# Kernel tuning notes

Measured on AMD Instinct MI355X. Metric: run time of the kernel, lower is better.

Reference implementation:

```python
import jax, jax.numpy as jnp
import numpy as np

B, C_CLS, D_WORD, J = 1024, 80, 300, 8000
IMG_CH = 2048

def setup_inputs() -> dict:
    key = jax.random.key(0)
    ks = jax.random.split(key, 9)
    return {
        'feature': jax.random.normal(ks[0], (B, IMG_CH), jnp.float32),
        'inp': jax.random.normal(ks[1], (1, C_CLS, D_WORD), jnp.float32),
        'A': jax.random.uniform(ks[2], (C_CLS, C_CLS), jnp.float32),
        'W_gc1': jax.random.normal(ks[3], (D_WORD, 1024), jnp.float32) * (1.0 / np.sqrt(1024)),
        'W_gc2': jax.random.normal(ks[4], (1024, 2048), jnp.float32) * (1.0 / np.sqrt(2048)),
        'W_img': jax.random.normal(ks[5], (J, IMG_CH), jnp.float32) * 0.02,
        'b_img': jax.random.normal(ks[6], (J,), jnp.float32) * 0.02,
        'W_cls': jax.random.normal(ks[7], (J, 2048), jnp.float32) * 0.02,
        'b_cls': jax.random.normal(ks[8], (J,), jnp.float32) * 0.02,
    }

def _gen_adj(A):
    # torch: D = A.sum(1)**-0.5; adj = (A @ diag(D)).T @ diag(D) = D[:,None]*A.T*D[None,:]
    D = jnp.power(jnp.sum(A, axis=1), -0.5)
    return D[:, None] * A.T * D[None, :]

def reference(feature, inp, A, W_gc1, W_gc2, W_img, b_img, W_cls, b_cls):
    inp0 = inp[0]                                   # [C, 300]
    adj = jax.lax.stop_gradient(_gen_adj(A))        # [C, C], .detach() in torch
    x = adj @ (inp0 @ W_gc1)                        # gc1: [C, 1024]
    x = jax.nn.leaky_relu(x, negative_slope=0.2)
    x = adj @ (x @ W_gc2)                           # gc2: [C, 2048]
    # MFB bilinear pooling (is_usemfb=True, is_hash=False -> out_in_tmp=1, eval-mode dropout=identity)
    # original: out[b,c] = sum_j (Linear_img(feature[b])[j] * Linear_cls(x_col_c)[j])
    img_proj = feature @ W_img.T + b_img            # [B, J]
    cls_proj = x @ W_cls.T + b_cls                  # [C, J]
    x_out = img_proj @ cls_proj.T                   # [B, C]
    return x_out
```

## Files before the change

kernel.cpp:

```cpp
#include <hip/hip_runtime.h>
#include <hip/hip_bf16.h>


typedef __bf16 bf16_t;
typedef __bf16 bf16x8 __attribute__((ext_vector_type(8)));
typedef float f32x4 __attribute__((ext_vector_type(4)));

#define MFMA16(a, b, c) __builtin_amdgcn_mfma_f32_16x16x32_bf16((a), (b), (c), 0, 0, 0)

__device__ inline bf16x8 cvt8(float4 a, float4 b) {
  bf16x8 v;
  v[0] = (bf16_t)a.x; v[1] = (bf16_t)a.y; v[2] = (bf16_t)a.z; v[3] = (bf16_t)a.w;
  v[4] = (bf16_t)b.x; v[5] = (bf16_t)b.y; v[6] = (bf16_t)b.z; v[7] = (bf16_t)b.w;
  return v;
}

__global__ void k_adj(const float* __restrict__ A, float* __restrict__ adj) {
  __shared__ float Dv[80];
  int tid = threadIdx.x;
  if (tid < 80) {
    float s = 0.f;
    #pragma unroll 4
    for (int j = 0; j < 80; ++j) s += A[tid * 80 + j];
    Dv[tid] = rsqrtf(s);
  }
  __syncthreads();
  for (int idx = tid; idx < 6400; idx += blockDim.x) {
    int i = idx / 80, j = idx % 80;
    adj[idx] = Dv[i] * Dv[j] * A[j * 80 + i];
  }
}

__global__ void k_cvt0(const float* __restrict__ inp0, bf16_t* __restrict__ x0b) {
  int idx = blockIdx.x * blockDim.x + threadIdx.x;
  if (idx < 30720) {
    int c = idx / 384, k = idx % 384;
    x0b[idx] = (k < 300) ? (bf16_t)inp0[c * 300 + k] : (bf16_t)0.f;
  }
}

__global__ __launch_bounds__(256) void k_gc1m(
    const bf16_t* __restrict__ x0b, const float* __restrict__ Wgc1,
    float* __restrict__ t1) {
  int tid = threadIdx.x;
  int w = tid >> 6, l = tid & 63;
  int ln = l & 15, q = l >> 4;
  int n0 = blockIdx.x * 16;

  __shared__ float red[4][80][16];
  f32x4 acc[5] = {};
  for (int ks = 0; ks < 3; ++ks) {
    int kq = w * 96 + ks * 32 + q * 8;
    bf16x8 bfrag;
    #pragma unroll
    for (int jj = 0; jj < 8; ++jj) {
      int k = kq + jj;
      int kc = k < 300 ? k : 299;
      float wv = Wgc1[kc * 1024 + n0 + ln];
      bfrag[jj] = (bf16_t)(k < 300 ? wv : 0.f);
    }
    #pragma unroll
    for (int mt = 0; mt < 5; ++mt) {
      bf16x8 afrag = *(const bf16x8*)(x0b + (size_t)(mt * 16 + ln) * 384 + kq);
      acc[mt] = MFMA16(afrag, bfrag, acc[mt]);
    }
  }
  #pragma unroll
  for (int mt = 0; mt < 5; ++mt)
    #pragma unroll
    for (int reg = 0; reg < 4; ++reg)
      red[w][mt * 16 + q * 4 + reg][ln] = acc[mt][reg];
  __syncthreads();
  for (int o = tid; o < 1280; o += 256) {
    int c = o >> 4, nn = o & 15;
    t1[c * 1024 + n0 + nn] = red[0][c][nn] + red[1][c][nn] + red[2][c][nn] + red[3][c][nn];
  }
}

__global__ void k_adjmul_leaky(const float* __restrict__ adj, const float* __restrict__ t1,
                               bf16_t* __restrict__ x1b) {
  int idx = blockIdx.x * blockDim.x + threadIdx.x;
  int c = idx >> 10, n = idx & 1023;
  const float* ar = adj + c * 80;
  float acc = 0.f;
  #pragma unroll 4
  for (int cc = 0; cc < 80; ++cc) acc += ar[cc] * t1[cc * 1024 + n];
  x1b[idx] = (bf16_t)(acc > 0.f ? acc : 0.2f * acc);
}

__global__ __launch_bounds__(256) void k_gc2m(
    const bf16_t* __restrict__ x1b, const float* __restrict__ Wgc2,
    float* __restrict__ t2) {
  int tid = threadIdx.x;
  int w = tid >> 6, l = tid & 63;
  int ln = l & 15, q = l >> 4;
  int nc = blockIdx.x & 31, kc = blockIdx.x >> 5;

  __shared__ float Bs[32][66];
  f32x4 acc[5] = {};
  for (int s = 0; s < 2; ++s) {
    int k0 = kc * 64 + s * 32;
    #pragma unroll
    for (int it = 0; it < 2; ++it) {
      int slot = tid + it * 256;
      int kr = slot >> 4, nq = slot & 15;
      const float4 v = *(const float4*)(Wgc2 + (size_t)(k0 + kr) * 2048 + nc * 64 + nq * 4);
      *(float4*)&Bs[kr][nq * 4] = v;
    }
    __syncthreads();
    bf16x8 bfrag;
    #pragma unroll
    for (int jj = 0; jj < 8; ++jj) bfrag[jj] = (bf16_t)Bs[q * 8 + jj][w * 16 + ln];
    #pragma unroll
    for (int mt = 0; mt < 5; ++mt) {
      bf16x8 afrag = *(const bf16x8*)(x1b + (size_t)(mt * 16 + ln) * 1024 + k0 + q * 8);
      acc[mt] = MFMA16(afrag, bfrag, acc[mt]);
    }
    __syncthreads();
  }
  #pragma unroll
  for (int mt = 0; mt < 5; ++mt)
    #pragma unroll
    for (int reg = 0; reg < 4; ++reg)
      atomicAdd(&t2[(size_t)(mt * 16 + q * 4 + reg) * 2048 + nc * 64 + w * 16 + ln],
                acc[mt][reg]);
}

__global__ void k_adjmul_bf16(const float* __restrict__ adj, const float* __restrict__ t2,
                              bf16_t* __restrict__ x2) {
  int idx = blockIdx.x * blockDim.x + threadIdx.x;
  int c = idx >> 11, n = idx & 2047;
  const float* ar = adj + c * 80;
  float acc = 0.f;
  #pragma unroll 4
  for (int cc = 0; cc < 80; ++cc) acc += ar[cc] * t2[cc * 2048 + n];
  x2[idx] = (bf16_t)acc;
}

__global__ __launch_bounds__(256) void k_clsproj(
    const float* __restrict__ Wcls, const float* __restrict__ bcls,
    const float* __restrict__ bimg, const bf16_t* __restrict__ x2,
    bf16_t* __restrict__ P, float* __restrict__ r) {
  int tid = threadIdx.x;
  int w = tid >> 6, l = tid & 63;
  int ln = l & 15, q = l >> 4;
  int j0 = blockIdx.x * 16;
  size_t jrow = (size_t)(j0 + ln) * 2048;

  __shared__ float red[4][80][16];
  __shared__ float rloc[80];
  if (tid < 80) rloc[tid] = 0.f;

  f32x4 acc[5] = {};
  int kbase = w * 512 + q * 8;
  for (int ks = 0; ks < 16; ++ks) {
    int kq = kbase + ks * 32;
    const float4* bp = (const float4*)(Wcls + jrow + kq);
    float4 b0 = bp[0], b1 = bp[1];
    bf16x8 bfrag = cvt8(b0, b1);
    #pragma unroll
    for (int mt = 0; mt < 5; ++mt) {
      bf16x8 afrag = *(const bf16x8*)(x2 + (size_t)(mt * 16 + ln) * 2048 + kq);
      acc[mt] = MFMA16(afrag, bfrag, acc[mt]);
    }
  }
  #pragma unroll
  for (int mt = 0; mt < 5; ++mt)
    #pragma unroll
    for (int reg = 0; reg < 4; ++reg)
      red[w][mt * 16 + q * 4 + reg][ln] = acc[mt][reg];
  __syncthreads();

  for (int o = tid; o < 1280; o += 256) {
    int c = o >> 4, jj = o & 15;
    float v = red[0][c][jj] + red[1][c][jj] + red[2][c][jj] + red[3][c][jj] + bcls[j0 + jj];
    P[(size_t)c * 8000 + j0 + jj] = (bf16_t)v;
    atomicAdd(&rloc[c], bimg[j0 + jj] * v);
  }
  __syncthreads();
  if (tid < 80) atomicAdd(&r[tid], rloc[tid]);
}

__global__ __launch_bounds__(256) void k_hmat(
    const float* __restrict__ Wimg, const bf16_t* __restrict__ P, float* __restrict__ H) {
  int tid = threadIdx.x;
  int w = tid >> 6, l = tid & 63;
  int ln = l & 15, q = l >> 4;
  int nc = blockIdx.x & 31, jc = blockIdx.x >> 5;

  __shared__ float Bs[32][66];
  f32x4 acc[5] = {};
  for (int s = 0; s < 10; ++s) {
    int j0 = jc * 320 + s * 32;
    #pragma unroll
    for (int it = 0; it < 2; ++it) {
      int slot = tid + it * 256;
      int jr = slot >> 4, nq = slot & 15;
      const float4 v = *(const float4*)(Wimg + (size_t)(j0 + jr) * 2048 + nc * 64 + nq * 4);
      *(float4*)&Bs[jr][nq * 4] = v;
    }
    __syncthreads();
    bf16x8 bfrag;
    #pragma unroll
    for (int jj = 0; jj < 8; ++jj) bfrag[jj] = (bf16_t)Bs[q * 8 + jj][w * 16 + ln];
    #pragma unroll
    for (int mt = 0; mt < 5; ++mt) {
      bf16x8 afrag = *(const bf16x8*)(P + (size_t)(mt * 16 + ln) * 8000 + j0 + q * 8);
      acc[mt] = MFMA16(afrag, bfrag, acc[mt]);
    }
    __syncthreads();
  }
  #pragma unroll
  for (int mt = 0; mt < 5; ++mt)
    #pragma unroll
    for (int reg = 0; reg < 4; ++reg)
      atomicAdd(&H[(size_t)(mt * 16 + q * 4 + reg) * 2048 + nc * 64 + w * 16 + ln],
                acc[mt][reg]);
}

__global__ __launch_bounds__(256) void k_out(
    const float* __restrict__ feat, const float* __restrict__ H,
    const float* __restrict__ r, float* __restrict__ out) {
  int tid = threadIdx.x;
  int w = tid >> 6, l = tid & 63;
  int ln = l & 15, q = l >> 4;
  int mg = blockIdx.x & 15, kc = blockIdx.x >> 4;
  int m0 = mg * 64 + w * 16;
  size_t frow = (size_t)(m0 + ln) * 2048;

  f32x4 acc[5] = {};
  int kbase = kc * 256 + q * 8;
  for (int ks = 0; ks < 8; ++ks) {
    int kq = kbase + ks * 32;
    const float4* ap = (const float4*)(feat + frow + kq);
    bf16x8 afrag = cvt8(ap[0], ap[1]);
    #pragma unroll
    for (int nt = 0; nt < 5; ++nt) {
      const float4* hp = (const float4*)(H + (size_t)(nt * 16 + ln) * 2048 + kq);
      bf16x8 bfrag = cvt8(hp[0], hp[1]);
      acc[nt] = MFMA16(afrag, bfrag, acc[nt]);
    }
  }
  #pragma unroll
  for (int nt = 0; nt < 5; ++nt)
    #pragma unroll
    for (int reg = 0; reg < 4; ++reg) {
      int b = m0 + q * 4 + reg;
      int c = nt * 16 + ln;
      float v = acc[nt][reg];
      if (kc == 0) v += r[c];
      atomicAdd(&out[b * 80 + c], v);
    }
}

extern "C" void kernel_launch(void* const* d_in, const int* in_sizes, int n_in,
                              void* d_out, int out_size, void* d_ws, size_t ws_size,
                              hipStream_t stream) {
  const float* feature = (const float*)d_in[0];
  const float* inp     = (const float*)d_in[1];
  const float* A       = (const float*)d_in[2];
  const float* Wgc1    = (const float*)d_in[3];
  const float* Wgc2    = (const float*)d_in[4];
  const float* Wimg    = (const float*)d_in[5];
  const float* bimg    = (const float*)d_in[6];
  const float* Wcls    = (const float*)d_in[7];
  const float* bcls    = (const float*)d_in[8];
  float* out = (float*)d_out;

  char* ws = (char*)d_ws;
  float*  adj = (float*)(ws + 0);
  float*  t1  = (float*)(ws + 25600);
  bf16_t* x1b = (bf16_t*)(ws + 353280);
  float*  t2  = (float*)(ws + 517120);
  bf16_t* x2  = (bf16_t*)(ws + 1172480);
  bf16_t* P   = (bf16_t*)(ws + 1500160);
  float*  H   = (float*)(ws + 2780160);
  float*  r   = (float*)(ws + 3435520);
  bf16_t* x0b = (bf16_t*)(ws + 3435840);

  hipMemsetAsync(t2, 0, 80 * 2048 * 4, stream);
  hipMemsetAsync(H, 0, 80 * 2048 * 4, stream);
  hipMemsetAsync(r, 0, 80 * 4, stream);
  hipMemsetAsync(out, 0, 1024 * 80 * 4, stream);

  k_adj<<<1, 128, 0, stream>>>(A, adj);
  k_cvt0<<<120, 256, 0, stream>>>(inp, x0b);
  k_gc1m<<<64, 256, 0, stream>>>(x0b, Wgc1, t1);
  k_adjmul_leaky<<<320, 256, 0, stream>>>(adj, t1, x1b);
  k_gc2m<<<512, 256, 0, stream>>>(x1b, Wgc2, t2);
  k_adjmul_bf16<<<640, 256, 0, stream>>>(adj, t2, x2);
  k_clsproj<<<500, 256, 0, stream>>>(Wcls, bcls, bimg, x2, P, r);
  k_hmat<<<800, 256, 0, stream>>>(Wimg, P, H);
  k_out<<<128, 256, 0, stream>>>(feature, H, r, out);
}
```

Before: 280.8 us.

## Pipeline weight tiles via direct global-to-LDS loads and split k_out K

k_gc2m and k_hmat now stage their fp32 weight tiles with global_load_lds into double- and triple-buffered shared memory. Explicit vmcnt waits and barriers let the next tile's loads overlap the current tile's MFMAs, and the A fragments are prefetched into registers. k_out splits K four times finer and launches 512 blocks instead of 128 to improve occupancy, at the cost of more output atomics. The hand-tuned vmcnt counts are fragile: a miscount could read stale LDS.

```diff
diff --git a/kernel.cpp b/kernel.cpp
--- a/kernel.cpp
+++ b/kernel.cpp
@@ -7,6 +7,24 @@
 typedef float f32x4 __attribute__((ext_vector_type(4)));
 
 #define MFMA16(a, b, c) __builtin_amdgcn_mfma_f32_16x16x32_bf16((a), (b), (c), 0, 0, 0)
+
+#define GLOAD_LDS16(g, l)                                     \
+  __builtin_amdgcn_global_load_lds(                           \
+      (const __attribute__((address_space(1))) void*)(g),     \
+      (__attribute__((address_space(3))) void*)(l), 16, 0, 0)
+
+#define PIN()                                   \
+  do {                                          \
+    asm volatile("" ::: "memory");              \
+    __builtin_amdgcn_sched_barrier(0);          \
+  } while (0)
+
+#define BARRIER()                               \
+  do {                                          \
+    PIN();                                      \
+    __builtin_amdgcn_s_barrier();               \
+    PIN();                                      \
+  } while (0)
 
 __device__ inline bf16x8 cvt8(float4 a, float4 b) {
   bf16x8 v;
@@ -96,28 +114,54 @@
   int ln = l & 15, q = l >> 4;
   int nc = blockIdx.x & 31, kc = blockIdx.x >> 5;
 
-  __shared__ float Bs[32][66];
-  f32x4 acc[5] = {};
-  for (int s = 0; s < 2; ++s) {
-    int k0 = kc * 64 + s * 32;
+  __shared__ float BsF[2 * 2048];
+  auto stage = [&](int b, int k0) {
     #pragma unroll
     for (int it = 0; it < 2; ++it) {
       int slot = tid + it * 256;
       int kr = slot >> 4, nq = slot & 15;
-      const float4 v = *(const float4*)(Wgc2 + (size_t)(k0 + kr) * 2048 + nc * 64 + nq * 4);
-      *(float4*)&Bs[kr][nq * 4] = v;
-    }
-    __syncthreads();
+      const float* src = Wgc2 + (size_t)(k0 + kr) * 2048 + nc * 64 + nq * 4;
+      float* dst = BsF + b * 2048 + slot * 4;
+      GLOAD_LDS16(src, dst);
+    }
+  };
+
+  int kb = kc * 64;
+  bf16x8 a0[5], a1[5];
+  #pragma unroll
+  for (int mt = 0; mt < 5; ++mt)
+    a0[mt] = *(const bf16x8*)(x1b + (size_t)(mt * 16 + ln) * 1024 + kb + q * 8);
+  PIN();
+  stage(0, kb);
+  PIN();
+  stage(1, kb + 32);
+  PIN();
+  #pragma unroll
+  for (int mt = 0; mt < 5; ++mt)
+    a1[mt] = *(const bf16x8*)(x1b + (size_t)(mt * 16 + ln) * 1024 + kb + 32 + q * 8);
+  PIN();
+
+  f32x4 acc[5] = {};
+  asm volatile("s_waitcnt vmcnt(7)" ::: "memory");
+  BARRIER();
+  {
     bf16x8 bfrag;
     #pragma unroll
-    for (int jj = 0; jj < 8; ++jj) bfrag[jj] = (bf16_t)Bs[q * 8 + jj][w * 16 + ln];
-    #pragma unroll
-    for (int mt = 0; mt < 5; ++mt) {
-      bf16x8 afrag = *(const bf16x8*)(x1b + (size_t)(mt * 16 + ln) * 1024 + k0 + q * 8);
-      acc[mt] = MFMA16(afrag, bfrag, acc[mt]);
-    }
-    __syncthreads();
-  }
+    for (int jj = 0; jj < 8; ++jj) bfrag[jj] = (bf16_t)BsF[(q * 8 + jj) * 64 + w * 16 + ln];
+    #pragma unroll
+    for (int mt = 0; mt < 5; ++mt) acc[mt] = MFMA16(a0[mt], bfrag, acc[mt]);
+  }
+  asm volatile("s_waitcnt vmcnt(5)" ::: "memory");
+  BARRIER();
+  {
+    bf16x8 bfrag;
+    #pragma unroll
+    for (int jj = 0; jj < 8; ++jj)
+      bfrag[jj] = (bf16_t)BsF[2048 + (q * 8 + jj) * 64 + w * 16 + ln];
+    #pragma unroll
+    for (int mt = 0; mt < 5; ++mt) acc[mt] = MFMA16(a1[mt], bfrag, acc[mt]);
+  }
+
   #pragma unroll
   for (int mt = 0; mt < 5; ++mt)
     #pragma unroll
@@ -187,29 +231,64 @@
   int w = tid >> 6, l = tid & 63;
   int ln = l & 15, q = l >> 4;
   int nc = blockIdx.x & 31, jc = blockIdx.x >> 5;
-
-  __shared__ float Bs[32][66];
-  f32x4 acc[5] = {};
-  for (int s = 0; s < 10; ++s) {
-    int j0 = jc * 320 + s * 32;
+  int jbase = jc * 320;
+
+  __shared__ float BsF[3 * 2048];
+
+  auto stage = [&](int b, int j0) {
     #pragma unroll
     for (int it = 0; it < 2; ++it) {
       int slot = tid + it * 256;
       int jr = slot >> 4, nq = slot & 15;
-      const float4 v = *(const float4*)(Wimg + (size_t)(j0 + jr) * 2048 + nc * 64 + nq * 4);
-      *(float4*)&Bs[jr][nq * 4] = v;
-    }
-    __syncthreads();
+      const float* src = Wimg + (size_t)(j0 + jr) * 2048 + nc * 64 + nq * 4;
+      float* dst = BsF + b * 2048 + slot * 4;
+      GLOAD_LDS16(src, dst);
+    }
+  };
+  auto loadA = [&](bf16x8* a, int j0) {
+    #pragma unroll
+    for (int mt = 0; mt < 5; ++mt)
+      a[mt] = *(const bf16x8*)(P + (size_t)(mt * 16 + ln) * 8000 + j0 + q * 8);
+  };
+
+  f32x4 acc[5] = {};
+  bf16x8 aCur[5], aNxt[5];
+
+  loadA(aCur, jbase);
+  PIN();
+  stage(0, jbase);
+  PIN();
+  stage(1, jbase + 32);
+  PIN();
+
+  #pragma unroll
+  for (int s = 0; s < 10; ++s) {
+    if (s < 9) {
+      loadA(aNxt, jbase + (s + 1) * 32);
+      PIN();
+    }
+    if (s < 8) {
+      stage((s + 2) % 3, jbase + (s + 2) * 32);
+      PIN();
+    }
+    if (s == 0)      asm volatile("s_waitcnt vmcnt(9)"  ::: "memory");
+    else if (s < 8)  asm volatile("s_waitcnt vmcnt(14)" ::: "memory");
+    else if (s == 8) asm volatile("s_waitcnt vmcnt(12)" ::: "memory");
+    else             asm volatile("s_waitcnt vmcnt(5)"  ::: "memory");
+    BARRIER();
+    const float* Bc = BsF + (s % 3) * 2048;
     bf16x8 bfrag;
     #pragma unroll
-    for (int jj = 0; jj < 8; ++jj) bfrag[jj] = (bf16_t)Bs[q * 8 + jj][w * 16 + ln];
-    #pragma unroll
-    for (int mt = 0; mt < 5; ++mt) {
-      bf16x8 afrag = *(const bf16x8*)(P + (size_t)(mt * 16 + ln) * 8000 + j0 + q * 8);
-      acc[mt] = MFMA16(afrag, bfrag, acc[mt]);
-    }
-    __syncthreads();
-  }
+    for (int jj = 0; jj < 8; ++jj) bfrag[jj] = (bf16_t)Bc[(q * 8 + jj) * 64 + w * 16 + ln];
+    #pragma unroll
+    for (int mt = 0; mt < 5; ++mt) acc[mt] = MFMA16(aCur[mt], bfrag, acc[mt]);
+    BARRIER();
+    if (s < 9) {
+      #pragma unroll
+      for (int mt = 0; mt < 5; ++mt) aCur[mt] = aNxt[mt];
+    }
+  }
+
   #pragma unroll
   for (int mt = 0; mt < 5; ++mt)
     #pragma unroll
@@ -229,8 +308,9 @@
   size_t frow = (size_t)(m0 + ln) * 2048;
 
   f32x4 acc[5] = {};
-  int kbase = kc * 256 + q * 8;
-  for (int ks = 0; ks < 8; ++ks) {
+  int kbase = kc * 64 + q * 8;
+  #pragma unroll
+  for (int ks = 0; ks < 2; ++ks) {
     int kq = kbase + ks * 32;
     const float4* ap = (const float4*)(feat + frow + kq);
     bf16x8 afrag = cvt8(ap[0], ap[1]);
@@ -291,5 +371,5 @@
   k_adjmul_bf16<<<640, 256, 0, stream>>>(adj, t2, x2);
   k_clsproj<<<500, 256, 0, stream>>>(Wcls, bcls, bimg, x2, P, r);
   k_hmat<<<800, 256, 0, stream>>>(Wimg, P, H);
-  k_out<<<128, 256, 0, stream>>>(feature, H, r, out);
-}
+  k_out<<<512, 256, 0, stream>>>(feature, H, r, out);
+}
```

New measurement: 278.6 us. Within noise of the previous version (-0.8%).
